# Kernel optimization log

Measured on AMD Instinct MI355X. Metric: run time of the kernel, lower is better.

Reference implementation:

```python
import jax, jax.numpy as jnp
import numpy as np

N = 50000
E = 800000
IN_C, HID_C, OUT_C = 128, 128, 40
K = 3  # PyG TAGConv default number of hops


def setup_inputs() -> dict:
    key = jax.random.key(0)
    k1, k2, k3, k4, k5, k6, k7 = jax.random.split(key, 7)
    x = jax.random.normal(k1, (N, IN_C), dtype=jnp.float32)
    edge_index = jax.random.randint(k2, (2, E), 0, N, dtype=jnp.int64)
    # Linear((K+1)*in, out) weights (stored as [in_total, out] for x @ W)
    s1 = 1.0 / np.sqrt((K + 1) * IN_C)
    s2 = 1.0 / np.sqrt((K + 1) * HID_C)
    W1 = jax.random.uniform(k3, ((K + 1) * IN_C, HID_C), jnp.float32, -s1, s1)
    b1 = jax.random.uniform(k4, (HID_C,), jnp.float32, -s1, s1)
    W2 = jax.random.uniform(k5, ((K + 1) * HID_C, OUT_C), jnp.float32, -s2, s2)
    b2 = jax.random.uniform(k6, (OUT_C,), jnp.float32, -s2, s2)
    return {"x": x, "edge_index": edge_index, "W1": W1, "b1": b1, "W2": W2, "b2": b2}


def _sym_norm(src, dst):
    # GCN-style symmetric normalization: deg computed on destination (col)
    deg = jax.ops.segment_sum(jnp.ones((E,), jnp.float32), dst, num_segments=N)
    dis = jnp.where(deg > 0, jax.lax.rsqrt(jnp.maximum(deg, 1.0)), 0.0)
    return dis[src] * dis[dst]  # [E]


def _tag_layer(x, src, dst, norm, W, b):
    xs = [x]
    h = x
    for _ in range(K):
        h = jax.ops.segment_sum(h[src] * norm[:, None], dst, num_segments=N)
        xs.append(h)
    return jnp.concatenate(xs, axis=1) @ W + b


def reference(x, edge_index, W1, b1, W2, b2):
    src, dst = edge_index[0], edge_index[1]
    norm = _sym_norm(src, dst)
    h = jax.nn.relu(_tag_layer(x, src, dst, norm, W1, b1))
    # F.dropout(training=False) is identity at inference
    h = _tag_layer(h, src, dst, norm, W2, b2)
    return jax.nn.log_softmax(h, axis=1)
```

## Files before the change

kernel.cpp:

```cpp
#include <hip/hip_runtime.h>
#include <hip/hip_bf16.h>

#define NNODES 50000
#define NROWP  50176
#define NEDGES 800000
#define KHOP 3
#define NBKT 196
#define BCAP 6144
#define ABLK 400
#define ACH  2000

typedef __attribute__((ext_vector_type(8))) short short8v;
typedef __attribute__((ext_vector_type(8))) __bf16 bf16x8;
typedef __attribute__((ext_vector_type(4))) float f32x4;

__device__ inline unsigned short f2bf(float f) {
  unsigned u = __builtin_bit_cast(unsigned, f);
  u += 0x7fffu + ((u >> 16) & 1u);
  return (unsigned short)(u >> 16);
}
__device__ inline float bflo(unsigned u) { return __builtin_bit_cast(float, u << 16); }
__device__ inline float bfhi(unsigned u) { return __builtin_bit_cast(float, u & 0xffff0000u); }

__device__ inline void gload_lds16(const void* g, void* l) {
  __builtin_amdgcn_global_load_lds(
      (const __attribute__((address_space(1))) unsigned int*)g,
      (__attribute__((address_space(3))) unsigned int*)l, 16, 0, 0);
}

__device__ inline f32x4 mfma_bf16(bf16x8 a, bf16x8 b, f32x4 c) {
  return __builtin_amdgcn_mfma_f32_16x16x32_bf16(a, b, c, 0, 0, 0);
}

__device__ inline void fma8(float* acc, float w, short8v v) {
  uint4 u = __builtin_bit_cast(uint4, v);
  acc[0] = fmaf(w, bflo(u.x), acc[0]);
  acc[1] = fmaf(w, bfhi(u.x), acc[1]);
  acc[2] = fmaf(w, bflo(u.y), acc[2]);
  acc[3] = fmaf(w, bfhi(u.y), acc[3]);
  acc[4] = fmaf(w, bflo(u.z), acc[4]);
  acc[5] = fmaf(w, bfhi(u.z), acc[5]);
  acc[6] = fmaf(w, bflo(u.w), acc[6]);
  acc[7] = fmaf(w, bfhi(u.w), acc[7]);
}

__device__ inline void fma4(float* acc, float w, uint2 v) {
  acc[0] = fmaf(w, bflo(v.x), acc[0]);
  acc[1] = fmaf(w, bfhi(v.x), acc[1]);
  acc[2] = fmaf(w, bflo(v.y), acc[2]);
  acc[3] = fmaf(w, bfhi(v.y), acc[3]);
}

__global__ __launch_bounds__(256) void bucketA_kernel(
    const int* __restrict__ src, const int* __restrict__ dst,
    int* __restrict__ bcur, int2* __restrict__ bkt) {
  __shared__ int2 eb[ACH];
  __shared__ int hist[256];
  __shared__ int base[256];
  int tid = threadIdx.x;
  int e0 = blockIdx.x * ACH;
  int cnt = NEDGES - e0; if (cnt > ACH) cnt = ACH;
  hist[tid] = 0;
  __syncthreads();
  for (int i = tid; i < cnt; i += 256) {
    int s = src[e0 + i], d = dst[e0 + i];
    eb[i] = make_int2(s, d);
    atomicAdd(&hist[d >> 8], 1);
  }
  __syncthreads();
  base[tid] = atomicAdd(&bcur[tid], hist[tid]);
  hist[tid] = 0;
  __syncthreads();
  for (int i = tid; i < cnt; i += 256) {
    int2 e = eb[i];
    int b = e.y >> 8;
    int off = atomicAdd(&hist[b], 1);
    bkt[(size_t)b * BCAP + base[b] + off] = e;
  }
}

__global__ __launch_bounds__(256) void bktscan_kernel(
    const int* __restrict__ bcur, int* __restrict__ boff, int* __restrict__ row_ptr) {
  __shared__ int sd[256];
  int tid = threadIdx.x;
  int own = (tid < NBKT) ? bcur[tid] : 0;
  sd[tid] = own;
  __syncthreads();
  for (int o = 1; o < 256; o <<= 1) {
    int t = (tid >= o) ? sd[tid - o] : 0;
    __syncthreads();
    sd[tid] += t;
    __syncthreads();
  }
  if (tid < NBKT) boff[tid] = sd[tid] - own;
  if (tid == 255) row_ptr[NNODES] = sd[255];
}

__global__ __launch_bounds__(256) void histC_kernel(
    const int* __restrict__ bcur, const int2* __restrict__ bkt,
    const int* __restrict__ boff, int* __restrict__ row_ptr,
    float* __restrict__ dis, int n) {
  __shared__ int h[256];
  __shared__ int sc[256];
  int b = blockIdx.x, tid = threadIdx.x;
  h[tid] = 0;
  __syncthreads();
  int sz = bcur[b];
  for (int i = tid; i < sz; i += 256)
    atomicAdd(&h[bkt[(size_t)b * BCAP + i].y & 255], 1);
  __syncthreads();
  int own = h[tid];
  sc[tid] = own;
  __syncthreads();
  for (int o = 1; o < 256; o <<= 1) {
    int t = (tid >= o) ? sc[tid - o] : 0;
    __syncthreads();
    sc[tid] += t;
    __syncthreads();
  }
  int node = b * 256 + tid;
  if (node < n) {
    row_ptr[node] = boff[b] + sc[tid] - own;
    dis[node] = (own > 0) ? rsqrtf((float)own) : 0.f;
  }
}

__global__ __launch_bounds__(256) void scatB_kernel(
    const int* __restrict__ bcur, const int2* __restrict__ bkt,
    const int* __restrict__ row_ptr, const float* __restrict__ dis,
    int2* __restrict__ csr, int n) {
  __shared__ int cur[256];
  int b = blockIdx.x, tid = threadIdx.x;
  int node = b * 256 + tid;
  cur[tid] = (node < n) ? row_ptr[node] : 0;
  __syncthreads();
  int sz = bcur[b];
  for (int i = tid; i < sz; i += 256) {
    int2 e = bkt[(size_t)b * BCAP + i];
    int pos = atomicAdd(&cur[e.y & 255], 1);
    int2 ent;
    ent.x = e.x;
    ent.y = __float_as_int(dis[e.x] * dis[e.y]);
    csr[pos] = ent;
  }
}

__global__ void wprep_kernel(const float* __restrict__ W1, const float* __restrict__ W2,
                             unsigned short* __restrict__ W1t,
                             unsigned short* __restrict__ W2pt) {
  int t = blockIdx.x * blockDim.x + threadIdx.x;
  if (t < 512 * 128) {
    int c = t >> 9, k = t & 511;
    W1t[t] = f2bf(W1[(size_t)k * 128 + c]);
  } else if (t < 512 * 128 + 160 * 128) {
    int u = t - 512 * 128;
    int q = u >> 7, r = u & 127;
    int k = q / 40, c = q - k * 40;
    W2pt[u] = f2bf(W2[(size_t)(k * 128 + r) * 40 + c]);
  }
}

__global__ void copyx_kernel(const float* __restrict__ x, unsigned short* __restrict__ P, int n) {
  int t = blockIdx.x * blockDim.x + threadIdx.x;
  int i = t >> 5;
  int c4 = (t & 31) << 2;
  if (i < n) {
    float4 v = *(const float4*)&x[(size_t)i * 128 + c4];
    unsigned lo = (unsigned)f2bf(v.x) | ((unsigned)f2bf(v.y) << 16);
    unsigned hi = (unsigned)f2bf(v.z) | ((unsigned)f2bf(v.w) << 16);
    uint2 o; o.x = lo; o.y = hi;
    *(uint2*)&P[(size_t)i * 512 + c4] = o;
  }
}

__global__ __launch_bounds__(256) void prop128c_kernel(
    const unsigned short* __restrict__ in, unsigned short* __restrict__ out,
    const int* __restrict__ row_ptr, const int2* __restrict__ csr, int n) {
  int node = (int)((blockIdx.x * blockDim.x + threadIdx.x) >> 6);
  int lane = threadIdx.x & 63;
  if (node >= n) return;
  int beg = row_ptr[node], end = row_ptr[node + 1];
  int deg = end - beg;
  int2 ent = make_int2(0, 0);
  if (lane < deg) ent = csr[beg + lane];
  const int grp = lane >> 4, sub = lane & 15;
  float acc[8] = {0.f, 0.f, 0.f, 0.f, 0.f, 0.f, 0.f, 0.f};
  int m = deg < 64 ? deg : 64;
  int j = 0;
  for (; j + 16 <= m; j += 16) {
    int s0 = __shfl(ent.x, j + grp, 64);
    float w0 = __int_as_float(__shfl(ent.y, j + grp, 64));
    int s1 = __shfl(ent.x, j + 4 + grp, 64);
    float w1 = __int_as_float(__shfl(ent.y, j + 4 + grp, 64));
    int s2 = __shfl(ent.x, j + 8 + grp, 64);
    float w2 = __int_as_float(__shfl(ent.y, j + 8 + grp, 64));
    int s3 = __shfl(ent.x, j + 12 + grp, 64);
    float w3 = __int_as_float(__shfl(ent.y, j + 12 + grp, 64));
    short8v v0 = *(const short8v*)(in + (size_t)s0 * 512 + sub * 8);
    short8v v1 = *(const short8v*)(in + (size_t)s1 * 512 + sub * 8);
    short8v v2 = *(const short8v*)(in + (size_t)s2 * 512 + sub * 8);
    short8v v3 = *(const short8v*)(in + (size_t)s3 * 512 + sub * 8);
    fma8(acc, w0, v0);
    fma8(acc, w1, v1);
    fma8(acc, w2, v2);
    fma8(acc, w3, v3);
  }
  for (; j + 8 <= m; j += 8) {
    int s0 = __shfl(ent.x, j + grp, 64);
    float w0 = __int_as_float(__shfl(ent.y, j + grp, 64));
    int s1 = __shfl(ent.x, j + 4 + grp, 64);
    float w1 = __int_as_float(__shfl(ent.y, j + 4 + grp, 64));
    short8v v0 = *(const short8v*)(in + (size_t)s0 * 512 + sub * 8);
    short8v v1 = *(const short8v*)(in + (size_t)s1 * 512 + sub * 8);
    fma8(acc, w0, v0);
    fma8(acc, w1, v1);
  }
  for (; j < m; j += 4) {
    int idx = j + grp;
    bool act = idx < m;
    int ic = act ? idx : m - 1;
    int s0 = __shfl(ent.x, ic, 64);
    float w0 = __int_as_float(__shfl(ent.y, ic, 64));
    if (!act) w0 = 0.f;
    short8v v0 = *(const short8v*)(in + (size_t)s0 * 512 + sub * 8);
    fma8(acc, w0, v0);
  }
  for (int t = beg + 64; t < end; ++t) {
    int2 e0 = csr[t];
    float w0 = (grp == 0) ? __int_as_float(e0.y) : 0.f;
    short8v v = *(const short8v*)(in + (size_t)e0.x * 512 + sub * 8);
    fma8(acc, w0, v);
  }
#pragma unroll
  for (int i = 0; i < 8; ++i) {
    acc[i] += __shfl_xor(acc[i], 16, 64);
    acc[i] += __shfl_xor(acc[i], 32, 64);
  }
  if (grp == 0) {
    uint4 r;
    r.x = (unsigned)f2bf(acc[0]) | ((unsigned)f2bf(acc[1]) << 16);
    r.y = (unsigned)f2bf(acc[2]) | ((unsigned)f2bf(acc[3]) << 16);
    r.z = (unsigned)f2bf(acc[4]) | ((unsigned)f2bf(acc[5]) << 16);
    r.w = (unsigned)f2bf(acc[6]) | ((unsigned)f2bf(acc[7]) << 16);
    *(uint4*)(out + (size_t)node * 512 + sub * 8) = r;
  }
}

__global__ __launch_bounds__(256) void gemm1m_kernel(
    const unsigned short* __restrict__ A,
    const unsigned short* __restrict__ Bt,
    const float* __restrict__ bias,
    unsigned short* __restrict__ H) {
  __shared__ short As[64 * 32];
  __shared__ short Bs[128 * 32];
  const int tid = threadIdx.x;
  const int lane = tid & 63;
  const int w = tid >> 6;
  const int wr = w & 1;
  const int wc = w >> 1;
  const int row0 = blockIdx.x * 64;
  f32x4 acc[2][4];
#pragma unroll
  for (int i = 0; i < 2; ++i)
#pragma unroll
    for (int j = 0; j < 4; ++j) acc[i][j] = (f32x4)0.f;

  const int lrow = lane >> 2;
  const int lkp = lane & 3;

  for (int k0 = 0; k0 < 512; k0 += 32) {
    gload_lds16(A + (size_t)(row0 + w * 16 + lrow) * 512 + k0 + lkp * 8, &As[w * 512]);
    gload_lds16(Bt + (size_t)(w * 16 + lrow) * 512 + k0 + lkp * 8, &Bs[w * 512]);
    gload_lds16(Bt + (size_t)((w + 4) * 16 + lrow) * 512 + k0 + lkp * 8, &Bs[(w + 4) * 512]);
    __syncthreads();
    const int kg = lane >> 4, rr = lane & 15;
    bf16x8 af[2], bfr[4];
#pragma unroll
    for (int mr = 0; mr < 2; ++mr)
      af[mr] = __builtin_bit_cast(bf16x8,
          *(const short8v*)&As[(wr * 32 + mr * 16 + rr) * 32 + kg * 8]);
#pragma unroll
    for (int nr = 0; nr < 4; ++nr)
      bfr[nr] = __builtin_bit_cast(bf16x8,
          *(const short8v*)&Bs[(wc * 64 + nr * 16 + rr) * 32 + kg * 8]);
#pragma unroll
    for (int mr = 0; mr < 2; ++mr)
#pragma unroll
      for (int nr = 0; nr < 4; ++nr)
        acc[mr][nr] = mfma_bf16(af[mr], bfr[nr], acc[mr][nr]);
    __syncthreads();
  }
  const int cg = lane >> 4, cl = lane & 15;
#pragma unroll
  for (int mr = 0; mr < 2; ++mr)
#pragma unroll
    for (int nr = 0; nr < 4; ++nr) {
      int col = wc * 64 + nr * 16 + cl;
      float bv = bias[col];
#pragma unroll
      for (int j = 0; j < 4; ++j) {
        int row = row0 + wr * 32 + mr * 16 + cg * 4 + j;
        H[(size_t)row * 128 + col] = f2bf(fmaxf(acc[mr][nr][j] + bv, 0.f));
      }
    }
}

__global__ __launch_bounds__(256) void gemm2m_kernel(
    const unsigned short* __restrict__ A,
    const unsigned short* __restrict__ Bt,
    unsigned short* __restrict__ G) {
  __shared__ short As[64 * 32];
  __shared__ short Bs[160 * 32];
  const int tid = threadIdx.x;
  const int lane = tid & 63;
  const int w = tid >> 6;
  const int row0 = blockIdx.x * 64;
  f32x4 acc[10];
#pragma unroll
  for (int i = 0; i < 10; ++i) acc[i] = (f32x4)0.f;
  const int lrow = lane >> 2, lkp = lane & 3;

  for (int k0 = 0; k0 < 128; k0 += 32) {
    gload_lds16(A + (size_t)(row0 + w * 16 + lrow) * 128 + k0 + lkp * 8, &As[w * 512]);
    for (int c = w; c < 10; c += 4)
      gload_lds16(Bt + (size_t)(c * 16 + lrow) * 128 + k0 + lkp * 8, &Bs[c * 512]);
    __syncthreads();
    const int kg = lane >> 4, rr = lane & 15;
    bf16x8 af = __builtin_bit_cast(bf16x8,
        *(const short8v*)&As[(w * 16 + rr) * 32 + kg * 8]);
#pragma unroll
    for (int nr = 0; nr < 10; ++nr) {
      bf16x8 bfr = __builtin_bit_cast(bf16x8,
          *(const short8v*)&Bs[(nr * 16 + rr) * 32 + kg * 8]);
      acc[nr] = mfma_bf16(af, bfr, acc[nr]);
    }
    __syncthreads();
  }
  const int cg = lane >> 4, cl = lane & 15;
#pragma unroll
  for (int nr = 0; nr < 10; ++nr) {
    int col = nr * 16 + cl;
    int k = col / 40;
    int o = col - k * 40;
#pragma unroll
    for (int j = 0; j < 4; ++j) {
      int row = row0 + w * 16 + cg * 4 + j;
      G[(size_t)k * NROWP * 64 + (size_t)row * 64 + o] = f2bf(acc[nr][j]);
    }
  }
}

__global__ __launch_bounds__(256) void prop40c_kernel(
    const unsigned short* __restrict__ in,
    const unsigned short* __restrict__ add,
    unsigned short* __restrict__ out,
    const int* __restrict__ row_ptr, const int2* __restrict__ csr, int n) {
  int node = (int)((blockIdx.x * blockDim.x + threadIdx.x) >> 6);
  int lane = threadIdx.x & 63;
  if (node >= n) return;
  int beg = row_ptr[node], end = row_ptr[node + 1];
  int deg = end - beg;
  int2 ent = make_int2(0, 0);
  if (lane < deg) ent = csr[beg + lane];
  const int grp = lane >> 4, sub = lane & 15;
  float acc[4] = {0.f, 0.f, 0.f, 0.f};
  if (grp == 0) {
    uint2 a = *(const uint2*)(add + (size_t)node * 64 + sub * 4);
    acc[0] = bflo(a.x); acc[1] = bfhi(a.x);
    acc[2] = bflo(a.y); acc[3] = bfhi(a.y);
  }
  int m = deg < 64 ? deg : 64;
  int j = 0;
  for (; j + 16 <= m; j += 16) {
    int s0 = __shfl(ent.x, j + grp, 64);
    float w0 = __int_as_float(__shfl(ent.y, j + grp, 64));
    int s1 = __shfl(ent.x, j + 4 + grp, 64);
    float w1 = __int_as_float(__shfl(ent.y, j + 4 + grp, 64));
    int s2 = __shfl(ent.x, j + 8 + grp, 64);
    float w2 = __int_as_float(__shfl(ent.y, j + 8 + grp, 64));
    int s3 = __shfl(ent.x, j + 12 + grp, 64);
    float w3 = __int_as_float(__shfl(ent.y, j + 12 + grp, 64));
    uint2 v0 = *(const uint2*)(in + (size_t)s0 * 64 + sub * 4);
    uint2 v1 = *(const uint2*)(in + (size_t)s1 * 64 + sub * 4);
    uint2 v2 = *(const uint2*)(in + (size_t)s2 * 64 + sub * 4);
    uint2 v3 = *(const uint2*)(in + (size_t)s3 * 64 + sub * 4);
    fma4(acc, w0, v0);
    fma4(acc, w1, v1);
    fma4(acc, w2, v2);
    fma4(acc, w3, v3);
  }
  for (; j + 8 <= m; j += 8) {
    int s0 = __shfl(ent.x, j + grp, 64);
    float w0 = __int_as_float(__shfl(ent.y, j + grp, 64));
    int s1 = __shfl(ent.x, j + 4 + grp, 64);
    float w1 = __int_as_float(__shfl(ent.y, j + 4 + grp, 64));
    uint2 v0 = *(const uint2*)(in + (size_t)s0 * 64 + sub * 4);
    uint2 v1 = *(const uint2*)(in + (size_t)s1 * 64 + sub * 4);
    fma4(acc, w0, v0);
    fma4(acc, w1, v1);
  }
  for (; j < m; j += 4) {
    int idx = j + grp;
    bool act = idx < m;
    int ic = act ? idx : m - 1;
    int s0 = __shfl(ent.x, ic, 64);
    float w0 = __int_as_float(__shfl(ent.y, ic, 64));
    if (!act) w0 = 0.f;
    uint2 v0 = *(const uint2*)(in + (size_t)s0 * 64 + sub * 4);
    fma4(acc, w0, v0);
  }
  for (int t = beg + 64; t < end; ++t) {
    int2 e0 = csr[t];
    float w = (grp == 0) ? __int_as_float(e0.y) : 0.f;
    uint2 v = *(const uint2*)(in + (size_t)e0.x * 64 + sub * 4);
    fma4(acc, w, v);
  }
#pragma unroll
  for (int i = 0; i < 4; ++i) {
    acc[i] += __shfl_xor(acc[i], 16, 64);
    acc[i] += __shfl_xor(acc[i], 32, 64);
  }
  if (grp == 0) {
    uint2 r;
    r.x = (unsigned)f2bf(acc[0]) | ((unsigned)f2bf(acc[1]) << 16);
    r.y = (unsigned)f2bf(acc[2]) | ((unsigned)f2bf(acc[3]) << 16);
    *(uint2*)(out + (size_t)node * 64 + sub * 4) = r;
  }
}

__global__ __launch_bounds__(256) void prop40c_lsm_kernel(
    const unsigned short* __restrict__ in,
    const unsigned short* __restrict__ add,
    const float* __restrict__ b2,
    float* __restrict__ out,
    const int* __restrict__ row_ptr, const int2* __restrict__ csr, int n) {
  int node = (int)((blockIdx.x * blockDim.x + threadIdx.x) >> 6);
  int lane = threadIdx.x & 63;
  if (node >= n) return;
  int beg = row_ptr[node], end = row_ptr[node + 1];
  int deg = end - beg;
  int2 ent = make_int2(0, 0);
  if (lane < deg) ent = csr[beg + lane];
  const int grp = lane >> 4, sub = lane & 15;
  float acc[4] = {0.f, 0.f, 0.f, 0.f};
  if (grp == 0) {
    uint2 a = *(const uint2*)(add + (size_t)node * 64 + sub * 4);
    acc[0] = bflo(a.x); acc[1] = bfhi(a.x);
    acc[2] = bflo(a.y); acc[3] = bfhi(a.y);
  }
  int m = deg < 64 ? deg : 64;
  int j = 0;
  for (; j + 16 <= m; j += 16) {
    int s0 = __shfl(ent.x, j + grp, 64);
    float w0 = __int_as_float(__shfl(ent.y, j + grp, 64));
    int s1 = __shfl(ent.x, j + 4 + grp, 64);
    float w1 = __int_as_float(__shfl(ent.y, j + 4 + grp, 64));
    int s2 = __shfl(ent.x, j + 8 + grp, 64);
    float w2 = __int_as_float(__shfl(ent.y, j + 8 + grp, 64));
    int s3 = __shfl(ent.x, j + 12 + grp, 64);
    float w3 = __int_as_float(__shfl(ent.y, j + 12 + grp, 64));
    uint2 v0 = *(const uint2*)(in + (size_t)s0 * 64 + sub * 4);
    uint2 v1 = *(const uint2*)(in + (size_t)s1 * 64 + sub * 4);
    uint2 v2 = *(const uint2*)(in + (size_t)s2 * 64 + sub * 4);
    uint2 v3 = *(const uint2*)(in + (size_t)s3 * 64 + sub * 4);
    fma4(acc, w0, v0);
    fma4(acc, w1, v1);
    fma4(acc, w2, v2);
    fma4(acc, w3, v3);
  }
  for (; j + 8 <= m; j += 8) {
    int s0 = __shfl(ent.x, j + grp, 64);
    float w0 = __int_as_float(__shfl(ent.y, j + grp, 64));
    int s1 = __shfl(ent.x, j + 4 + grp, 64);
    float w1 = __int_as_float(__shfl(ent.y, j + 4 + grp, 64));
    uint2 v0 = *(const uint2*)(in + (size_t)s0 * 64 + sub * 4);
    uint2 v1 = *(const uint2*)(in + (size_t)s1 * 64 + sub * 4);
    fma4(acc, w0, v0);
    fma4(acc, w1, v1);
  }
  for (; j < m; j += 4) {
    int idx = j + grp;
    bool act = idx < m;
    int ic = act ? idx : m - 1;
    int s0 = __shfl(ent.x, ic, 64);
    float w0 = __int_as_float(__shfl(ent.y, ic, 64));
    if (!act) w0 = 0.f;
    uint2 v0 = *(const uint2*)(in + (size_t)s0 * 64 + sub * 4);
    fma4(acc, w0, v0);
  }
  for (int t = beg + 64; t < end; ++t) {
    int2 e0 = csr[t];
    float w = (grp == 0) ? __int_as_float(e0.y) : 0.f;
    uint2 v = *(const uint2*)(in + (size_t)e0.x * 64 + sub * 4);
    fma4(acc, w, v);
  }
#pragma unroll
  for (int i = 0; i < 4; ++i) {
    acc[i] += __shfl_xor(acc[i], 16, 64);
    acc[i] += __shfl_xor(acc[i], 32, 64);
  }
  bool val = (sub < 10);
  float vv[4];
  if (val) {
    float4 bv = *(const float4*)(b2 + sub * 4);
    vv[0] = acc[0] + bv.x; vv[1] = acc[1] + bv.y;
    vv[2] = acc[2] + bv.z; vv[3] = acc[3] + bv.w;
  } else {
    vv[0] = vv[1] = vv[2] = vv[3] = -__builtin_inff();
  }
  float mx = fmaxf(fmaxf(vv[0], vv[1]), fmaxf(vv[2], vv[3]));
#pragma unroll
  for (int o = 1; o < 16; o <<= 1) mx = fmaxf(mx, __shfl_xor(mx, o, 64));
  float s = 0.f;
  if (val)
    s = expf(vv[0] - mx) + expf(vv[1] - mx) + expf(vv[2] - mx) + expf(vv[3] - mx);
#pragma unroll
  for (int o = 1; o < 16; o <<= 1) s += __shfl_xor(s, o, 64);
  if (grp == 0 && val) {
    float ls = logf(s);
    float4 o4;
    o4.x = vv[0] - mx - ls; o4.y = vv[1] - mx - ls;
    o4.z = vv[2] - mx - ls; o4.w = vv[3] - mx - ls;
    *(float4*)(out + (size_t)node * 40 + sub * 4) = o4;
  }
}

extern "C" void kernel_launch(void* const* d_in, const int* in_sizes, int n_in,
                              void* d_out, int out_size, void* d_ws, size_t ws_size,
                              hipStream_t stream) {
  const float* x  = (const float*)d_in[0];
  const int*   ei = (const int*)d_in[1];
  const float* W1 = (const float*)d_in[2];
  const float* b1 = (const float*)d_in[3];
  const float* W2 = (const float*)d_in[4];
  const float* b2 = (const float*)d_in[5];
  const int* srcv = ei;
  const int* dstv = ei + NEDGES;
  float* out = (float*)d_out;

  char* wsb = (char*)d_ws;
  size_t off = 0;
  auto alloc = [&](size_t bytes) {
    char* p = wsb + off;
    off += (bytes + 255) & ~(size_t)255;
    return p;
  };
  float*          dis     = (float*)          alloc((size_t)NNODES * 4);
  int*            row_ptr = (int*)            alloc(((size_t)NNODES + 1) * 4);
  int*            bcur    = (int*)            alloc((size_t)256 * 4);
  int*            boff    = (int*)            alloc((size_t)NBKT * 4);
  int2*           bkt     = (int2*)           alloc((size_t)NBKT * BCAP * 8);
  int2*           csr     = (int2*)           alloc((size_t)NEDGES * 8);
  unsigned short* W1t     = (unsigned short*) alloc((size_t)128 * 512 * 2);
  unsigned short* W2pt    = (unsigned short*) alloc((size_t)160 * 128 * 2);
  unsigned short* P       = (unsigned short*) alloc((size_t)NROWP * 512 * 2);
  unsigned short* H       = (unsigned short*) alloc((size_t)NROWP * 128 * 2);
  unsigned short* G       = (unsigned short*) alloc((size_t)4 * NROWP * 64 * 2);
  unsigned short* tb      = (unsigned short*) alloc((size_t)NNODES * 64 * 2);
  unsigned short* t2      = (unsigned short*) alloc((size_t)NNODES * 64 * 2);

  unsigned short* G0 = G;
  unsigned short* G1 = G + (size_t)1 * NROWP * 64;
  unsigned short* G2 = G + (size_t)2 * NROWP * 64;
  unsigned short* G3 = G + (size_t)3 * NROWP * 64;

  hipMemsetAsync(bcur, 0, 256 * 4, stream);
  bucketA_kernel<<<ABLK, 256, 0, stream>>>(srcv, dstv, bcur, bkt);
  bktscan_kernel<<<1, 256, 0, stream>>>(bcur, boff, row_ptr);
  histC_kernel<<<NBKT, 256, 0, stream>>>(bcur, bkt, boff, row_ptr, dis, NNODES);
  scatB_kernel<<<NBKT, 256, 0, stream>>>(bcur, bkt, row_ptr, dis, csr, NNODES);
  wprep_kernel<<<(512 * 128 + 160 * 128 + 255) / 256, 256, 0, stream>>>(W1, W2, W1t, W2pt);
  copyx_kernel<<<((NNODES * 32) + 255) / 256, 256, 0, stream>>>(x, P, NNODES);

  const int prop_blocks = (NNODES * 64 + 255) / 256;
  for (int k = 1; k <= KHOP; ++k)
    prop128c_kernel<<<prop_blocks, 256, 0, stream>>>(P + 128 * (k - 1), P + 128 * k,
                                                     row_ptr, csr, NNODES);
  const int gemm_blocks = (NNODES + 63) / 64;
  gemm1m_kernel<<<gemm_blocks, 256, 0, stream>>>(P, W1t, b1, H);
  gemm2m_kernel<<<gemm_blocks, 256, 0, stream>>>(H, W2pt, G);
  prop40c_kernel<<<prop_blocks, 256, 0, stream>>>(G3, G2, tb, row_ptr, csr, NNODES);
  prop40c_kernel<<<prop_blocks, 256, 0, stream>>>(tb, G1, t2, row_ptr, csr, NNODES);
  prop40c_lsm_kernel<<<prop_blocks, 256, 0, stream>>>(t2, G0, b2, out, row_ptr, csr, NNODES);
}
```

Measured before the change: 229.9 us.

## Fuse first and second layer GEMMs, keeping hidden tile in LDS

Merges the two GEMM kernels into one. The ReLU'd hidden tile stays in shared memory with padded rows and feeds the second-layer projection directly, so the hidden activations are no longer written to and read back from global memory, and one launch goes away. Shared memory is reused for the W2 staging after the first GEMM. LDS use per block rises, which may lower occupancy. It also changes the edge-bucketing launch to twice as many blocks, each with half-size chunks.

```diff
diff --git a/kernel.cpp b/kernel.cpp
--- a/kernel.cpp
+++ b/kernel.cpp
@@ -7,8 +7,8 @@
 #define KHOP 3
 #define NBKT 196
 #define BCAP 6144
-#define ABLK 400
-#define ACH  2000
+#define ABLK 800
+#define ACH  1000
 
 typedef __attribute__((ext_vector_type(8))) short short8v;
 typedef __attribute__((ext_vector_type(8))) __bf16 bf16x8;
@@ -246,34 +246,38 @@
   }
 }
 
-__global__ __launch_bounds__(256) void gemm1m_kernel(
+__global__ __launch_bounds__(256) void gemm12_kernel(
     const unsigned short* __restrict__ A,
-    const unsigned short* __restrict__ Bt,
+    const unsigned short* __restrict__ B1t,
     const float* __restrict__ bias,
-    unsigned short* __restrict__ H) {
-  __shared__ short As[64 * 32];
-  __shared__ short Bs[128 * 32];
+    const unsigned short* __restrict__ B2t,
+    unsigned short* __restrict__ G) {
+  __shared__ short smem[2048 + 4096 + 64 * 136];
+  short* As  = smem;
+  short* Bs1 = smem + 2048;
+  short* Ht  = smem + 2048 + 4096;
+  short* Bs2c = smem;
   const int tid = threadIdx.x;
   const int lane = tid & 63;
   const int w = tid >> 6;
   const int wr = w & 1;
   const int wc = w >> 1;
   const int row0 = blockIdx.x * 64;
-  f32x4 acc[2][4];
-#pragma unroll
-  for (int i = 0; i < 2; ++i)
-#pragma unroll
-    for (int j = 0; j < 4; ++j) acc[i][j] = (f32x4)0.f;
-
   const int lrow = lane >> 2;
   const int lkp = lane & 3;
+  const int kg = lane >> 4, rr = lane & 15;
+
+  f32x4 acc[2][4];
+#pragma unroll
+  for (int i = 0; i < 2; ++i)
+#pragma unroll
+    for (int j = 0; j < 4; ++j) acc[i][j] = (f32x4)0.f;
 
   for (int k0 = 0; k0 < 512; k0 += 32) {
     gload_lds16(A + (size_t)(row0 + w * 16 + lrow) * 512 + k0 + lkp * 8, &As[w * 512]);
-    gload_lds16(Bt + (size_t)(w * 16 + lrow) * 512 + k0 + lkp * 8, &Bs[w * 512]);
-    gload_lds16(Bt + (size_t)((w + 4) * 16 + lrow) * 512 + k0 + lkp * 8, &Bs[(w + 4) * 512]);
-    __syncthreads();
-    const int kg = lane >> 4, rr = lane & 15;
+    gload_lds16(B1t + (size_t)(w * 16 + lrow) * 512 + k0 + lkp * 8, &Bs1[w * 512]);
+    gload_lds16(B1t + (size_t)((w + 4) * 16 + lrow) * 512 + k0 + lkp * 8, &Bs1[(w + 4) * 512]);
+    __syncthreads();
     bf16x8 af[2], bfr[4];
 #pragma unroll
     for (int mr = 0; mr < 2; ++mr)
@@ -282,7 +286,7 @@
 #pragma unroll
     for (int nr = 0; nr < 4; ++nr)
       bfr[nr] = __builtin_bit_cast(bf16x8,
-          *(const short8v*)&Bs[(wc * 64 + nr * 16 + rr) * 32 + kg * 8]);
+          *(const short8v*)&Bs1[(wc * 64 + nr * 16 + rr) * 32 + kg * 8]);
 #pragma unroll
     for (int mr = 0; mr < 2; ++mr)
 #pragma unroll
@@ -290,62 +294,53 @@
         acc[mr][nr] = mfma_bf16(af[mr], bfr[nr], acc[mr][nr]);
     __syncthreads();
   }
-  const int cg = lane >> 4, cl = lane & 15;
-#pragma unroll
-  for (int mr = 0; mr < 2; ++mr)
-#pragma unroll
-    for (int nr = 0; nr < 4; ++nr) {
-      int col = wc * 64 + nr * 16 + cl;
-      float bv = bias[col];
-#pragma unroll
-      for (int j = 0; j < 4; ++j) {
-        int row = row0 + wr * 32 + mr * 16 + cg * 4 + j;
-        H[(size_t)row * 128 + col] = f2bf(fmaxf(acc[mr][nr][j] + bv, 0.f));
+  {
+    const int cg = lane >> 4, cl = lane & 15;
+#pragma unroll
+    for (int mr = 0; mr < 2; ++mr)
+#pragma unroll
+      for (int nr = 0; nr < 4; ++nr) {
+        int col = wc * 64 + nr * 16 + cl;
+        float bv = bias[col];
+#pragma unroll
+        for (int j = 0; j < 4; ++j) {
+          int lr = wr * 32 + mr * 16 + cg * 4 + j;
+          Ht[lr * 136 + col] = (short)f2bf(fmaxf(acc[mr][nr][j] + bv, 0.f));
+        }
       }
-    }
-}
-
-__global__ __launch_bounds__(256) void gemm2m_kernel(
-    const unsigned short* __restrict__ A,
-    const unsigned short* __restrict__ Bt,
-    unsigned short* __restrict__ G) {
-  __shared__ short As[64 * 32];
-  __shared__ short Bs[160 * 32];
-  const int tid = threadIdx.x;
-  const int lane = tid & 63;
-  const int w = tid >> 6;
-  const int row0 = blockIdx.x * 64;
-  f32x4 acc[10];
-#pragma unroll
-  for (int i = 0; i < 10; ++i) acc[i] = (f32x4)0.f;
-  const int lrow = lane >> 2, lkp = lane & 3;
+  }
+  __syncthreads();
+
+  f32x4 acc2[10];
+#pragma unroll
+  for (int i = 0; i < 10; ++i) acc2[i] = (f32x4)0.f;
 
   for (int k0 = 0; k0 < 128; k0 += 32) {
-    gload_lds16(A + (size_t)(row0 + w * 16 + lrow) * 128 + k0 + lkp * 8, &As[w * 512]);
     for (int c = w; c < 10; c += 4)
-      gload_lds16(Bt + (size_t)(c * 16 + lrow) * 128 + k0 + lkp * 8, &Bs[c * 512]);
-    __syncthreads();
-    const int kg = lane >> 4, rr = lane & 15;
+      gload_lds16(B2t + (size_t)(c * 16 + lrow) * 128 + k0 + lkp * 8, &Bs2c[c * 512]);
+    __syncthreads();
     bf16x8 af = __builtin_bit_cast(bf16x8,
-        *(const short8v*)&As[(w * 16 + rr) * 32 + kg * 8]);
+        *(const short8v*)&Ht[(w * 16 + rr) * 136 + k0 + kg * 8]);
 #pragma unroll
     for (int nr = 0; nr < 10; ++nr) {
       bf16x8 bfr = __builtin_bit_cast(bf16x8,
-          *(const short8v*)&Bs[(nr * 16 + rr) * 32 + kg * 8]);
-      acc[nr] = mfma_bf16(af, bfr, acc[nr]);
+          *(const short8v*)&Bs2c[(nr * 16 + rr) * 32 + kg * 8]);
+      acc2[nr] = mfma_bf16(af, bfr, acc2[nr]);
     }
     __syncthreads();
   }
-  const int cg = lane >> 4, cl = lane & 15;
-#pragma unroll
-  for (int nr = 0; nr < 10; ++nr) {
-    int col = nr * 16 + cl;
-    int k = col / 40;
-    int o = col - k * 40;
-#pragma unroll
-    for (int j = 0; j < 4; ++j) {
-      int row = row0 + w * 16 + cg * 4 + j;
-      G[(size_t)k * NROWP * 64 + (size_t)row * 64 + o] = f2bf(acc[nr][j]);
+  {
+    const int cg = lane >> 4, cl = lane & 15;
+#pragma unroll
+    for (int nr = 0; nr < 10; ++nr) {
+      int col = nr * 16 + cl;
+      int k = col / 40;
+      int o = col - k * 40;
+#pragma unroll
+      for (int j = 0; j < 4; ++j) {
+        int row = row0 + w * 16 + cg * 4 + j;
+        G[(size_t)k * NROWP * 64 + (size_t)row * 64 + o] = f2bf(acc2[nr][j]);
+      }
     }
   }
 }
@@ -554,7 +549,6 @@
   unsigned short* W1t     = (unsigned short*) alloc((size_t)128 * 512 * 2);
   unsigned short* W2pt    = (unsigned short*) alloc((size_t)160 * 128 * 2);
   unsigned short* P       = (unsigned short*) alloc((size_t)NROWP * 512 * 2);
-  unsigned short* H       = (unsigned short*) alloc((size_t)NROWP * 128 * 2);
   unsigned short* G       = (unsigned short*) alloc((size_t)4 * NROWP * 64 * 2);
   unsigned short* tb      = (unsigned short*) alloc((size_t)NNODES * 64 * 2);
   unsigned short* t2      = (unsigned short*) alloc((size_t)NNODES * 64 * 2);
@@ -577,8 +571,7 @@
     prop128c_kernel<<<prop_blocks, 256, 0, stream>>>(P + 128 * (k - 1), P + 128 * k,
                                                      row_ptr, csr, NNODES);
   const int gemm_blocks = (NNODES + 63) / 64;
-  gemm1m_kernel<<<gemm_blocks, 256, 0, stream>>>(P, W1t, b1, H);
-  gemm2m_kernel<<<gemm_blocks, 256, 0, stream>>>(H, W2pt, G);
+  gemm12_kernel<<<gemm_blocks, 256, 0, stream>>>(P, W1t, b1, W2pt, G);
   prop40c_kernel<<<prop_blocks, 256, 0, stream>>>(G3, G2, tb, row_ptr, csr, NNODES);
   prop40c_kernel<<<prop_blocks, 256, 0, stream>>>(tb, G1, t2, row_ptr, csr, NNODES);
   prop40c_lsm_kernel<<<prop_blocks, 256, 0, stream>>>(t2, G0, b2, out, row_ptr, csr, NNODES);
```

New measurement: 229.6 us, median of 2. No clear change (-0.1%).
